# Kernel tuning notes

Hardware: AMD Instinct MI355X
Metric: run time of the kernel (lower is better)

## Reference

```python
import jax, jax.numpy as jnp
import numpy as np
import itertools

# ---- static config (from args) ----
BS = 4; H = 480; W = 640; C = 20
RES = 5; ZRES = 5; MAP_SZ = 480            # map_size_cm//global_downscaling//resolution
VR = 100; FOV = 79.0; NSEM = 16; NC = 1 + NSEM
MAXH = 40; MINH = -8; NZ = MAXH - MINH      # 48 z slices
AGENT_H = 88.0                              # camera_height*100
CAT_T = 5.0; EXP_T = 1.0; MAP_T = 1.0
RADIUS = 30
MIN_Z = int(25 / ZRES - MINH)               # 13
MID_Z = int(AGENT_H / ZRES - MINH)          # 25
MAX_Z = int((AGENT_H + 50) / ZRES - MINH)   # 35
R2D = 57.29577951308232

_F = (W / 2.0) / np.tan(np.deg2rad(FOV / 2.0))
_XC = (W - 1.0) / 2.0
_ZC = (H - 1.0) / 2.0

# circular stair mask (constant)
_ii, _jj = np.meshgrid(np.arange(2 * RADIUS), np.arange(2 * RADIUS), indexing='ij')
STAIR_MASK = jnp.asarray((((_ii + 0.5 - RADIUS) ** 2 + (_jj + 0.5 - RADIUS) ** 2) <= RADIUS ** 2).astype(np.float32))


def affine_grid(theta, Hh, Ww):
    # F.affine_grid, align_corners=False: sample at pixel centers
    xs = (jnp.arange(Ww, dtype=theta.dtype) + 0.5) * 2.0 / Ww - 1.0
    ys = (jnp.arange(Hh, dtype=theta.dtype) + 0.5) * 2.0 / Hh - 1.0
    gx, gy = jnp.meshgrid(xs, ys)  # [H,W]
    base = jnp.stack([gx, gy, jnp.ones_like(gx)], -1)  # [H,W,3]
    return jnp.einsum('hwk,bjk->bhwj', base, theta)    # [B,H,W,2]


def grid_sample(im, grid):
    # F.grid_sample: bilinear, align_corners=True, zeros padding
    B, Cc, Hh, Ww = im.shape
    x = (grid[..., 0] + 1.0) * 0.5 * (Ww - 1)
    y = (grid[..., 1] + 1.0) * 0.5 * (Hh - 1)
    x0 = jnp.floor(x); y0 = jnp.floor(y)

    def gather(ix, iy):
        valid = ((ix >= 0) & (ix < Ww) & (iy >= 0) & (iy < Hh)).astype(im.dtype)
        ixc = jnp.clip(ix, 0, Ww - 1).astype(jnp.int32)
        iyc = jnp.clip(iy, 0, Hh - 1).astype(jnp.int32)
        v = jax.vmap(lambda imb, iyb, ixb: imb[:, iyb, ixb])(im, iyc, ixc)  # [B,C,Hg,Wg]
        return v * valid[:, None, :, :]

    wx = x - x0; wy = y - y0
    return (gather(x0, y0) * ((1 - wx) * (1 - wy))[:, None]
            + gather(x0 + 1, y0) * (wx * (1 - wy))[:, None]
            + gather(x0, y0 + 1) * ((1 - wx) * wy)[:, None]
            + gather(x0 + 1, y0 + 1) * (wx * wy)[:, None])


def splat_feat_nd(feat, coords, dims):
    # trilinear scatter-add splat; feat [B,F,N], coords [B,3,N] in [-1,1]
    B, Fc, N = feat.shape
    G = int(np.prod(dims))
    grid = jnp.zeros((B, Fc, G), feat.dtype)
    pos, wts = [], []
    for d, D in enumerate(dims):
        p = coords[:, d, :] * (D / 2.0) + D / 2.0
        fl = jnp.floor(p)
        pd, wd = [], []
        for ix in (0, 1):
            pix = fl + ix
            safe = ((pix > 0) & (pix < D)).astype(p.dtype)
            wd.append((1.0 - jnp.abs(p - pix)) * safe)
            pd.append(pix * safe)
        pos.append(pd); wts.append(wd)

    def scat(g, idx, val):
        return jax.vmap(lambda gb, ib, vb: gb.at[:, ib].add(vb))(g, idx, val)

    for c0, c1, c2 in itertools.product((0, 1), repeat=3):
        idx = ((pos[0][c0] * dims[1] + pos[1][c1]) * dims[2] + pos[2][c2]).astype(jnp.int32)
        w = wts[0][c0] * wts[1][c1] * wts[2][c2]
        grid = scat(grid, idx, feat * w[:, None, :])
    return jnp.round(grid).reshape(B, Fc, *dims)


def maxpool3(x):  # 3x3 stride1 pad1 max pool, [B,1,H,W]
    return jax.lax.reduce_window(x, -jnp.inf, jax.lax.max, (1, 1, 3, 3), (1, 1, 1, 1), 'SAME')


def _forward(obs, pose_obs, maps_last, poses_last, eve_angle):
    bs, c, h, w = obs.shape
    depth = obs[:, 3]  # [B,H,W], cm

    # point cloud from depth (grid_z flipped top->bottom as in du)
    gx = jnp.arange(w, dtype=obs.dtype)[None, None, :]
    gz = jnp.arange(h - 1, -1, -1, dtype=obs.dtype)[None, :, None]
    X = (gx - _XC) * depth / _F
    Zc = (gz - _ZC) * depth / _F

    # camera elevation rotation about x-axis (per env) + sensor height
    a = jnp.deg2rad(eve_angle)[:, None, None]
    ca, sa = jnp.cos(a), jnp.sin(a)
    Y = ca * depth - sa * Zc
    Z = sa * depth + ca * Zc + AGENT_H
    X = X + VR * RES / 2.0  # shift_loc (rotation angle is 0)

    # normalize to [-1,1] voxel coords
    xs = (X / RES - VR // 2) / VR * 2.0
    ys = (Y / RES - VR // 2) / VR * 2.0
    zs = (Z / ZRES - (MAXH + MINH) // 2) / (MAXH - MINH) * 2.0
    coords = jnp.stack([xs, ys, zs], 1).reshape(bs, 3, h * w)

    feat = jnp.concatenate([jnp.ones((bs, 1, h * w), obs.dtype),
                            obs[:, 4:].reshape(bs, c - 4, h * w)], 1)  # du_scale=1 -> avgpool is identity

    voxels = splat_feat_nd(feat, coords, (VR, VR, NZ)).transpose(0, 1, 3, 2, 4)  # [B,F,y,x,z]

    ahp = voxels[..., MIN_Z:MAX_Z].sum(-1)
    asp = voxels[..., MID_Z - 5:MID_Z].sum(-1)
    allp = voxels.sum(-1)

    fp_map = jnp.clip(ahp[:, 0:1] / MAP_T, 0.0, 1.0)
    fp_stair = jnp.clip(asp[:, 0:1] / MAP_T, 0.0, 1.0)
    fp_exp = jnp.clip(allp[:, 0:1] / EXP_T, 0.0, 1.0)

    x1 = MAP_SZ // 2 - VR // 2; x2 = x1 + VR
    y1 = MAP_SZ // 2; y2 = y1 + VR
    agent_view = jnp.zeros((bs, c, MAP_SZ, MAP_SZ), obs.dtype)
    agent_view = agent_view.at[:, 0:1, y1:y2, x1:x2].set(fp_map)
    agent_view = agent_view.at[:, 1:2, y1:y2, x1:x2].set(fp_exp)
    agent_view = agent_view.at[:, 4:, y1:y2, x1:x2].set(jnp.clip(ahp[:, 1:] / CAT_T, 0.0, 1.0))
    agent_view_stair = jax.lax.stop_gradient(agent_view).at[:, 0:1, y1:y2, x1:x2].set(fp_stair)

    # pose composition (get_new_pose_batch)
    r = poses_last[:, 2] / R2D
    ny = poses_last[:, 1] + pose_obs[:, 0] * jnp.sin(r) + pose_obs[:, 1] * jnp.cos(r)
    nx = poses_last[:, 0] + pose_obs[:, 0] * jnp.cos(r) - pose_obs[:, 1] * jnp.sin(r)
    nt = poses_last[:, 2] + pose_obs[:, 2] * R2D
    nt = jnp.fmod(nt - 180.0, 360.0) + 180.0
    nt = jnp.fmod(nt + 180.0, 360.0) - 180.0
    current_poses = jnp.stack([nx, ny, nt], 1)

    stp = jax.lax.stop_gradient(current_poses)  # st_pose detached in source
    half = MAP_SZ // 2
    sx = (half - stp[:, 0] * 100.0 / RES) / half
    sy = (half - stp[:, 1] * 100.0 / RES) / half
    t = jnp.deg2rad(90.0 - stp[:, 2])
    ct, st = jnp.cos(t), jnp.sin(t)
    zero = jnp.zeros_like(ct); one = jnp.ones_like(ct)
    theta1 = jnp.stack([jnp.stack([ct, -st, zero], 1), jnp.stack([st, ct, zero], 1)], 1)
    theta2 = jnp.stack([jnp.stack([one, zero, sx], 1), jnp.stack([zero, one, sy], 1)], 1)
    rot_grid = affine_grid(theta1, MAP_SZ, MAP_SZ)
    trans_grid = affine_grid(theta2, MAP_SZ, MAP_SZ)

    translated = grid_sample(grid_sample(agent_view, rot_grid), trans_grid)

    diff = translated[:, 1:2] - maxpool3(translated[:, 0:1])
    diff = (diff > 0.8).astype(obs.dtype)
    map_pred = jnp.maximum(maps_last, translated)
    kill = (diff == 1.0) & (eve_angle == 0.0)[:, None, None, None]
    map_pred = map_pred.at[:, 0:1].set(jnp.where(kill, 0.0, map_pred[:, 0:1]))

    translated_stair = grid_sample(grid_sample(agent_view_stair, rot_grid), trans_grid)
    s_x = jnp.clip((current_poses[0, 0] * 100.0 / 5.0).astype(jnp.int32), RADIUS, MAP_SZ - RADIUS - 1)
    s_y = jnp.clip((current_poses[0, 1] * 100.0 / 5.0).astype(jnp.int32), RADIUS, MAP_SZ - RADIUS - 1)
    stair_grid = jax.lax.dynamic_update_slice(jnp.zeros((MAP_SZ, MAP_SZ), obs.dtype), STAIR_MASK,
                                              (s_y - RADIUS, s_x - RADIUS))
    translated_stair = translated_stair.at[0, 0:2].multiply(stair_grid[None])

    diff_s = translated_stair[:, 1:2] - translated_stair[:, 0:1]
    diff_s = (diff_s > 0.8).astype(obs.dtype)
    map_pred_stair = jnp.maximum(maps_last, translated_stair)
    kill_s = (diff_s == 1.0) & (eve_angle == 0.0)[:, None, None, None]
    map_pred_stair = map_pred_stair.at[:, 0:1].set(jnp.where(kill_s, 0.0, map_pred_stair[:, 0:1]))

    return translated, map_pred, map_pred_stair, current_poses


def setup_inputs() -> dict:
    key = jax.random.key(0)
    k1, k2, k3, k4, k5 = jax.random.split(key, 5)
    obs = jax.random.uniform(k1, (BS, C, H, W), jnp.float32)
    depth = jax.random.uniform(k2, (BS, H, W), jnp.float32) * 400.0 + 50.0  # cm
    obs = obs.at[:, 3].set(depth)
    pose_obs = (jax.random.uniform(k3, (BS, 3), jnp.float32) - 0.5) * 0.2   # small rel pose (m, m, rad)
    maps_last = jax.random.uniform(k4, (BS, C, MAP_SZ, MAP_SZ), jnp.float32)
    poses_last = jnp.tile(jnp.array([12.0, 12.0, 0.0], jnp.float32), (BS, 1)) \
        + (jax.random.uniform(k5, (BS, 3), jnp.float32) - 0.5) * jnp.array([2.0, 2.0, 60.0], jnp.float32)
    eve_angle = jnp.array([0.0, -30.0, 0.0, 30.0], jnp.float32)
    return {"obs": obs, "pose_obs": pose_obs, "maps_last": maps_last,
            "poses_last": poses_last, "eve_angle": eve_angle}


def reference(obs, pose_obs, maps_last, poses_last, eve_angle):
    return _forward(obs, pose_obs, maps_last, poses_last, eve_angle)
```

## Files before the change

kernel.cpp:

```cpp
#include <hip/hip_runtime.h>
#include <math.h>

#define BS 4
#define NCH 20
#define IMH 480
#define IMW 640
#define NPIX (IMH*IMW)
#define MSZ 480
#define MPX (MSZ*MSZ)
#define VR 100

#define TX 5
#define TY 8
#define NRX 20
#define NRY 13
#define NBIN (NRX*NRY)
#define CELLS (TX*TY)
#define CELLF 401

#define WND 176
#define NT  11

#define FPSCALE 65536.0f
#define FPINV   (1.0f/65536.0f)
#define SEMSCALE 65535.0f
#define SEMINV   (1.0f/65535.0f)

#define FCONST 388.19028f
#define D2R    0.017453292519943295f
#define R2DF   57.29577951308232f

typedef float    fx4  __attribute__((ext_vector_type(4)));
typedef unsigned ux4  __attribute__((ext_vector_type(4)));

static constexpr size_t SEG = (size_t)BS*NCH*MPX;
static constexpr size_t SEMT_FLOATS = (size_t)BS*NPIX*8;
static constexpr size_t LIST_CAP    = (size_t)4*BS*NPIX;
static constexpr size_t LIST_OFF_OUT = SEMT_FLOATS;
static_assert(LIST_OFF_OUT + LIST_CAP < 2*SEG, "semT+list must fit in out0+out1 segments");

static constexpr size_t OFF_AV     = 0;
static constexpr size_t OFF_AVS    = 720000;
static constexpr size_t OFF_COUNTS = 1681664;
static constexpr size_t OFF_CURS   = 1682704;
static constexpr size_t OFF_OFFS   = 1683744;
static constexpr size_t OFF_SEMT   = 1684800;
static constexpr size_t OFF_LIST   = OFF_SEMT + SEMT_FLOATS;
static constexpr size_t WS_NEED_B  = (OFF_LIST + LIST_CAP) * 4;

__device__ __forceinline__ float clip01(float v) { return fminf(fmaxf(v, 0.0f), 1.0f); }

struct Geo { float px, py, pz; };

__device__ __forceinline__ Geo geom(int p, float depth, float ca, float sa) {
  int j = p % IMW;
  int i = p / IMW;
  float dF = depth * (1.0f / FCONST);
  float X  = ((float)j - 319.5f) * dF;
  X += 250.0f;
  float gz = (float)(IMH - 1 - i);
  float Zc = (gz - 239.5f) * dF;
  float Y  = ca*depth - sa*Zc;
  float Z  = sa*depth + ca*Zc + 88.0f;
  float xs = (X/5.0f - 50.0f)/100.0f*2.0f;
  float ys = (Y/5.0f - 50.0f)/100.0f*2.0f;
  float zs = (Z/5.0f - 16.0f)/48.0f*2.0f;
  Geo g;
  g.px = xs*50.0f + 50.0f;
  g.py = ys*50.0f + 50.0f;
  g.pz = zs*24.0f + 24.0f;
  return g;
}

__device__ __forceinline__ int pixel_bins(Geo g, int bins[4]) {
  float fx = floorf(g.px), fy = floorf(g.py), fz = floorf(g.pz);
  float fx1 = fx + 1.0f, fy1 = fy + 1.0f, fz1 = fz + 1.0f;
  bool vx0 = (fx  > 0.0f) && (fx  < 100.0f);
  bool vx1 = (fx1 > 0.0f) && (fx1 < 100.0f);
  bool vy0 = (fy  > 0.0f) && (fy  < 100.0f);
  bool vy1 = (fy1 > 0.0f) && (fy1 < 100.0f);
  bool vz0 = (fz  > 0.0f) && (fz  < 48.0f);
  bool vz1 = (fz1 > 0.0f) && (fz1 < 48.0f);
  if (!((vx0||vx1) && (vy0||vy1) && (vz0||vz1))) return 0;
  int rxs[2]; int nx = 0;
  if (vx0) rxs[nx++] = (int)fx / TX;
  if (vx1) { int r = (int)fx1 / TX; if (!nx || r != rxs[0]) rxs[nx++] = r; }
  int rys[2]; int ny = 0;
  if (vy0) rys[ny++] = (int)fy / TY;
  if (vy1) { int r = (int)fy1 / TY; if (!ny || r != rys[0]) rys[ny++] = r; }
  int n = 0;
  for (int a = 0; a < ny; ++a)
    for (int c = 0; c < nx; ++c)
      bins[n++] = rys[a]*NRX + rxs[c];
  return n;
}

__device__ __forceinline__ void pose_calc(const float* __restrict__ pose_obs,
                                          const float* __restrict__ poses_last,
                                          int b, float& nx, float& ny, float& nt) {
  float pl0 = poses_last[b*3+0], pl1 = poses_last[b*3+1], pl2 = poses_last[b*3+2];
  float po0 = pose_obs[b*3+0],   po1 = pose_obs[b*3+1],   po2 = pose_obs[b*3+2];
  float r  = pl2 / R2DF;
  float sr = sinf(r), cr = cosf(r);
  ny = pl1 + po0*sr + po1*cr;
  nx = pl0 + po0*cr - po1*sr;
  nt = pl2 + po2*R2DF;
  nt = fmodf(nt - 180.0f, 360.0f) + 180.0f;
  nt = fmodf(nt + 180.0f, 360.0f) - 180.0f;
}

__global__ __launch_bounds__(256) void k_prep(const float* __restrict__ obs,
                                              const float* __restrict__ pose_obs,
                                              const float* __restrict__ poses_last,
                                              const float* __restrict__ eve,
                                              unsigned* __restrict__ counts,
                                              unsigned short* __restrict__ semT,
                                              float* __restrict__ out_poses) {
  __shared__ unsigned hist[NBIN];
  int tid = threadIdx.x;
  int b   = blockIdx.y;
  if (blockIdx.x == 0 && b == 0 && tid < BS) {
    float nx, ny, nt;
    pose_calc(pose_obs, poses_last, tid, nx, ny, nt);
    out_poses[tid*3+0] = nx;
    out_poses[tid*3+1] = ny;
    out_poses[tid*3+2] = nt;
  }
  for (int i = tid; i < NBIN; i += 256) hist[i] = 0u;
  __syncthreads();
  float a  = eve[b] * D2R;
  float ca = cosf(a), sa = sinf(a);
  const float* __restrict__ dpl  = obs + ((size_t)b*NCH + 3)*NPIX;
  const float* __restrict__ semb = obs + ((size_t)b*NCH + 4)*NPIX;
  int base = blockIdx.x * 2048;
#pragma unroll
  for (int k = 0; k < 8; ++k) {
    int p = base + k*256 + tid;
    Geo g = geom(p, dpl[p], ca, sa);
    int bins[4];
    int n = pixel_bins(g, bins);
    for (int t = 0; t < n; ++t) atomicAdd(&hist[bins[t]], 1u);
    bool wantSem = false;
    if (n > 0) {
      float fz = floorf(g.pz);
#pragma unroll
      for (int kk = 0; kk < 2; ++kk) {
        float pv = fz + (float)kk;
        if (pv > 0.0f && pv < 48.0f) {
          int zv = (int)pv;
          if (zv >= 13 && zv < 35) wantSem = true;
        }
      }
    }
    if (wantSem) {
      unsigned u[8];
#pragma unroll
      for (int k2 = 0; k2 < 8; ++k2) {
        float s0 = semb[(size_t)(2*k2  )*NPIX + p];
        float s1 = semb[(size_t)(2*k2+1)*NPIX + p];
        unsigned q0 = (unsigned)(clip01(s0)*SEMSCALE + 0.5f);
        unsigned q1 = (unsigned)(clip01(s1)*SEMSCALE + 0.5f);
        u[k2] = q0 | (q1 << 16);
      }
      ux4* dst = (ux4*)(semT + ((size_t)b*NPIX + p)*16);
      ux4 v0 = {u[0], u[1], u[2], u[3]};
      ux4 v1 = {u[4], u[5], u[6], u[7]};
      __builtin_nontemporal_store(v0, dst);
      __builtin_nontemporal_store(v1, dst + 1);
    }
  }
  __syncthreads();
  for (int i = tid; i < NBIN; i += 256) {
    unsigned v = hist[i];
    if (v) atomicAdd(&counts[b*NBIN + i], v);
  }
}

__global__ __launch_bounds__(256) void k_scatter(const float* __restrict__ obs,
                                                 const float* __restrict__ eve,
                                                 const unsigned* __restrict__ counts,
                                                 unsigned* __restrict__ curs,
                                                 unsigned* __restrict__ offs_g,
                                                 unsigned* __restrict__ list) {
  __shared__ unsigned hist[NBIN];
  __shared__ unsigned lbase[NBIN];
  __shared__ unsigned slot[NBIN];
  __shared__ unsigned offsL[BS*NBIN];
  __shared__ unsigned partial[256];
  int tid = threadIdx.x;
  int b   = blockIdx.y;
  for (int i = tid; i < NBIN; i += 256) { hist[i] = 0u; slot[i] = 0u; }
  {
    unsigned loc[5]; unsigned s = 0;
#pragma unroll
    for (int k = 0; k < 5; ++k) {
      int idx = tid*5 + k;
      unsigned v = (idx < BS*NBIN) ? counts[idx] : 0u;
      loc[k] = s; s += v;
    }
    partial[tid] = s;
    __syncthreads();
    for (int off = 1; off < 256; off <<= 1) {
      unsigned v = (tid >= off) ? partial[tid - off] : 0u;
      __syncthreads();
      partial[tid] += v;
      __syncthreads();
    }
    unsigned base = (tid > 0) ? partial[tid-1] : 0u;
#pragma unroll
    for (int k = 0; k < 5; ++k) {
      int idx = tid*5 + k;
      if (idx < BS*NBIN) offsL[idx] = base + loc[k];
    }
    __syncthreads();
  }
  if (blockIdx.x == 0 && b == 0)
    for (int i = tid; i < BS*NBIN; i += 256) offs_g[i] = offsL[i];

  float a  = eve[b] * D2R;
  float ca = cosf(a), sa = sinf(a);
  const float* __restrict__ dpl = obs + ((size_t)b*NCH + 3)*NPIX;
  int base = blockIdx.x * 2048;
#pragma unroll
  for (int k = 0; k < 8; ++k) {
    int p = base + k*256 + tid;
    Geo g = geom(p, dpl[p], ca, sa);
    int bins[4];
    int n = pixel_bins(g, bins);
    for (int t = 0; t < n; ++t) atomicAdd(&hist[bins[t]], 1u);
  }
  __syncthreads();
  for (int i = tid; i < NBIN; i += 256) {
    unsigned h = hist[i];
    lbase[i] = h ? (offsL[b*NBIN + i] + atomicAdd(&curs[b*NBIN + i], h)) : 0u;
  }
  __syncthreads();
#pragma unroll
  for (int k = 0; k < 8; ++k) {
    int p = base + k*256 + tid;
    Geo g = geom(p, dpl[p], ca, sa);
    int bins[4];
    int n = pixel_bins(g, bins);
    for (int t = 0; t < n; ++t) {
      int bn = bins[t];
      unsigned sidx = atomicAdd(&slot[bn], 1u);
      list[lbase[bn] + sidx] = (unsigned)p;
    }
  }
}

__global__ __launch_bounds__(1024) void k_splat_fast(const float* __restrict__ obs,
                                                     const unsigned short* __restrict__ semT,
                                                     const float* __restrict__ eve,
                                                     const unsigned* __restrict__ offs,
                                                     const unsigned* __restrict__ counts,
                                                     const unsigned* __restrict__ list,
                                                     float* __restrict__ av,
                                                     float* __restrict__ avs,
                                                     const float* __restrict__ maps_last,
                                                     float* __restrict__ out0,
                                                     float* __restrict__ out1,
                                                     float* __restrict__ out2,
                                                     int nSplat, int nFast) {
  __shared__ unsigned lds[CELLS * CELLF];
  const int bid = blockIdx.x;
  const int tid = threadIdx.x;

  if (bid >= nSplat) {
    const size_t n4 = SEG/4;
    const size_t stride = (size_t)nFast * 1024;
    const fx4* __restrict__ m4 = (const fx4*)maps_last;
    fx4 z4 = {0.0f, 0.0f, 0.0f, 0.0f};
    for (size_t i = (size_t)(bid - nSplat) * 1024 + tid; i < n4; i += stride) {
      fx4 m = __builtin_nontemporal_load(m4 + i);
      fx4 r;
      r.x = fmaxf(m.x, 0.0f); r.y = fmaxf(m.y, 0.0f);
      r.z = fmaxf(m.z, 0.0f); r.w = fmaxf(m.w, 0.0f);
      __builtin_nontemporal_store(z4, (fx4*)out0 + i);
      __builtin_nontemporal_store(r,  (fx4*)out1 + i);
      __builtin_nontemporal_store(r,  (fx4*)out2 + i);
    }
    return;
  }

  const int reg = bid % NBIN;
  const int b   = bid / NBIN;
  const int rx0 = (reg % NRX) * TX;
  const int ry0 = (reg / NRX) * TY;

  for (int i = tid; i < CELLS * CELLF; i += 1024) lds[i] = 0u;
  __syncthreads();

  float aa = eve[b] * D2R;
  float ca = cosf(aa), sa = sinf(aa);
  const float* __restrict__ dpl = obs + ((size_t)b*NCH + 3)*NPIX;

  const unsigned bin   = (unsigned)b*NBIN + reg;
  const unsigned start = offs[bin];
  const unsigned n     = counts[bin];

  for (unsigned ii = tid; ii < n; ii += 1024) {
    int p = (int)list[start + ii];
    Geo g = geom(p, dpl[p], ca, sa);
    float px = g.px, py = g.py, pz = g.pz;
    float fx = floorf(px), fy = floorf(py), fz = floorf(pz);

    float wxa[2], wya[2], wza[2];
    int   ixa[2], iya[2], iza[2];
    bool  vx[2], vy[2], vz[2];
#pragma unroll
    for (int k = 0; k < 2; ++k) {
      float pv = fx + (float)k;
      bool sg = (pv > 0.0f) && (pv < 100.0f);
      wxa[k] = sg ? (1.0f - fabsf(px - pv)) : 0.0f;
      ixa[k] = (int)pv;
      vx[k]  = sg && (ixa[k] >= rx0) && (ixa[k] < rx0 + TX);

      pv = fy + (float)k;
      sg = (pv > 0.0f) && (pv < 100.0f);
      wya[k] = sg ? (1.0f - fabsf(py - pv)) : 0.0f;
      iya[k] = (int)pv;
      vy[k]  = sg && (iya[k] >= ry0) && (iya[k] < ry0 + TY);

      pv = fz + (float)k;
      sg = (pv > 0.0f) && (pv < 48.0f);
      wza[k] = sg ? (1.0f - fabsf(pz - pv)) : 0.0f;
      iza[k] = (int)pv;
      vz[k]  = sg;
    }

    bool needSem = false;
#pragma unroll
    for (int k = 0; k < 2; ++k)
      if (vz[k] && iza[k] >= 13 && iza[k] < 35 && wza[k] != 0.0f) needSem = true;

    float sem[16];
    if (needSem) {
      const ux4* sp = (const ux4*)(semT + ((size_t)b*NPIX + p)*16);
      ux4 a4 = sp[0], b4 = sp[1];
      sem[0]  = (float)(a4.x & 0xffffu); sem[1]  = (float)(a4.x >> 16);
      sem[2]  = (float)(a4.y & 0xffffu); sem[3]  = (float)(a4.y >> 16);
      sem[4]  = (float)(a4.z & 0xffffu); sem[5]  = (float)(a4.z >> 16);
      sem[6]  = (float)(a4.w & 0xffffu); sem[7]  = (float)(a4.w >> 16);
      sem[8]  = (float)(b4.x & 0xffffu); sem[9]  = (float)(b4.x >> 16);
      sem[10] = (float)(b4.y & 0xffffu); sem[11] = (float)(b4.y >> 16);
      sem[12] = (float)(b4.z & 0xffffu); sem[13] = (float)(b4.z >> 16);
      sem[14] = (float)(b4.w & 0xffffu); sem[15] = (float)(b4.w >> 16);
    }

#pragma unroll
    for (int cx = 0; cx < 2; ++cx) {
      if (!vx[cx] || wxa[cx] == 0.0f) continue;
#pragma unroll
      for (int cy = 0; cy < 2; ++cy) {
        if (!vy[cy]) continue;
        float wxy = wxa[cx] * wya[cy];
        if (wxy == 0.0f) continue;
        unsigned* cellp = lds + (size_t)((ixa[cx]-rx0)*TY + (iya[cy]-ry0)) * CELLF;
#pragma unroll
        for (int cz = 0; cz < 2; ++cz) {
          if (!vz[cz]) continue;
          float wv = wxy * wza[cz];
          if (wv == 0.0f) continue;
          int zv = iza[cz];
          atomicAdd(cellp + zv, (unsigned)(wv*FPSCALE + 0.5f));
          if (zv >= 13 && zv < 35) {
            unsigned* p2 = cellp + 48 + (zv - 13)*16;
#pragma unroll
            for (int c = 0; c < 16; ++c)
              atomicAdd(p2 + c, (unsigned)(wv*sem[c] + 0.5f));
          }
        }
      }
    }
  }
  __syncthreads();

  for (int it = tid; it < CELLS * 17; it += 1024) {
    int cell = it % CELLS;
    int ch   = it / CELLS;
    int lx = cell / TY, ly = cell % TY;
    int x = rx0 + lx, y = ry0 + ly;
    if (y >= 100) continue;
    size_t pxo = (size_t)y*VR + x;
    size_t ab  = (size_t)b*18*10000;
    const unsigned* cellp = lds + (size_t)cell * CELLF;
    if (ch == 0) {
      float all0 = 0.0f, ahp0 = 0.0f, asp0 = 0.0f;
#pragma unroll
      for (int z = 0; z < 48; ++z) {
        float v = rintf((float)cellp[z] * FPINV);
        all0 += v;
        if (z >= 13 && z < 35) ahp0 += v;
        if (z >= 20 && z < 25) asp0 += v;
      }
      av[ab + 0*10000 + pxo] = clip01(ahp0);
      av[ab + 1*10000 + pxo] = clip01(all0);
      avs[(size_t)b*10000 + pxo] = clip01(asp0);
    } else {
      int c = ch - 1;
      float acc = 0.0f;
      for (int z = 0; z < 22; ++z) acc += rintf((float)cellp[48 + z*16 + c] * SEMINV);
      av[ab + (size_t)(2 + c)*10000 + pxo] = clip01(acc / 5.0f);
    }
  }
}

__global__ __launch_bounds__(256) void k_fast(const float* __restrict__ maps_last,
                                              float* __restrict__ out0,
                                              float* __restrict__ out1,
                                              float* __restrict__ out2) {
  const size_t n4 = SEG/4;
  const size_t stride = (size_t)gridDim.x * 256;
  const fx4* __restrict__ m4 = (const fx4*)maps_last;
  fx4 z4 = {0.0f, 0.0f, 0.0f, 0.0f};
  for (size_t i = (size_t)blockIdx.x * 256 + threadIdx.x; i < n4; i += stride) {
    fx4 m = __builtin_nontemporal_load(m4 + i);
    fx4 r;
    r.x = fmaxf(m.x, 0.0f); r.y = fmaxf(m.y, 0.0f);
    r.z = fmaxf(m.z, 0.0f); r.w = fmaxf(m.w, 0.0f);
    __builtin_nontemporal_store(z4, (fx4*)out0 + i);
    __builtin_nontemporal_store(r,  (fx4*)out1 + i);
    __builtin_nontemporal_store(r,  (fx4*)out2 + i);
  }
}

struct Nb { float wt, w00, w10, w01, w11; int o00, o10, o01, o11; };

__device__ __forceinline__ Nb rot_taps(int xi, int yi, float ct, float st, float wt) {
  Nb nb; nb.wt = 0.0f;
  nb.w00 = nb.w10 = nb.w01 = nb.w11 = 0.0f;
  nb.o00 = nb.o10 = nb.o01 = nb.o11 = 0;
  if (xi < 0 || xi >= MSZ || yi < 0 || yi >= MSZ) return nb;
  float gx = ((xi + 0.5f)*2.0f)/480.0f - 1.0f;
  float gy = ((yi + 0.5f)*2.0f)/480.0f - 1.0f;
  float u = gx*ct - gy*st;
  float v = gx*st + gy*ct;
  float xf = (u + 1.0f)*0.5f*479.0f;
  float yf = (v + 1.0f)*0.5f*479.0f;
  float x0f = floorf(xf), y0f = floorf(yf);
  int x0 = (int)x0f, y0 = (int)y0f;
  if (x0 < 189 || x0 > 289 || y0 < 239 || y0 > 339) return nb;
  float wx = xf - x0f, wy = yf - y0f;
  bool vx0 = (x0   >= 190) && (x0   < 290);
  bool vx1 = (x0+1 >= 190) && (x0+1 < 290);
  bool vy0 = (y0   >= 240) && (y0   < 340);
  bool vy1 = (y0+1 >= 240) && (y0+1 < 340);
  int base = (y0-240)*100 + (x0-190);
  bool v00 = vx0&&vy0, v10 = vx1&&vy0, v01 = vx0&&vy1, v11 = vx1&&vy1;
  nb.w00 = v00 ? (1.0f-wx)*(1.0f-wy) : 0.0f;  nb.o00 = v00 ? base       : 0;
  nb.w10 = v10 ? wx*(1.0f-wy)        : 0.0f;  nb.o10 = v10 ? base + 1   : 0;
  nb.w01 = v01 ? (1.0f-wx)*wy        : 0.0f;  nb.o01 = v01 ? base + 100 : 0;
  nb.w11 = v11 ? wx*wy               : 0.0f;  nb.o11 = v11 ? base + 101 : 0;
  nb.wt  = wt;
  return nb;
}

__device__ __forceinline__ bool trans_nbs(int w, int h, float sx, float sy,
                                          float ct, float st, Nb nb[4]) {
#pragma unroll
  for (int i = 0; i < 4; ++i) {
    nb[i].wt = 0.0f;
    nb[i].w00 = nb[i].w10 = nb[i].w01 = nb[i].w11 = 0.0f;
    nb[i].o00 = nb[i].o10 = nb[i].o01 = nb[i].o11 = 0;
  }
  float gx = ((w + 0.5f)*2.0f)/480.0f - 1.0f;
  float gy = ((h + 0.5f)*2.0f)/480.0f - 1.0f;
  float xf = ((gx + sx) + 1.0f)*0.5f*479.0f;
  float yf = ((gy + sy) + 1.0f)*0.5f*479.0f;
  float x0f = floorf(xf), y0f = floorf(yf);
  int x0 = (int)x0f, y0 = (int)y0f;
  if (x0 < -1 || x0 > 479 || y0 < -1 || y0 > 479) return false;
  float wx = xf - x0f, wy = yf - y0f;
  nb[0] = rot_taps(x0,   y0,   ct, st, (1.0f-wx)*(1.0f-wy));
  nb[1] = rot_taps(x0+1, y0,   ct, st, wx*(1.0f-wy));
  nb[2] = rot_taps(x0,   y0+1, ct, st, (1.0f-wx)*wy);
  nb[3] = rot_taps(x0+1, y0+1, ct, st, wx*wy);
  return (nb[0].wt!=0.0f)||(nb[1].wt!=0.0f)||(nb[2].wt!=0.0f)||(nb[3].wt!=0.0f);
}

__device__ __forceinline__ float eval_plane(const float* __restrict__ plane, const Nb nb[4]) {
  float t = 0.0f;
#pragma unroll
  for (int i = 0; i < 4; ++i) {
    if (nb[i].wt == 0.0f) continue;
    float r = plane[nb[i].o00]*nb[i].w00 + plane[nb[i].o10]*nb[i].w10
            + plane[nb[i].o01]*nb[i].w01 + plane[nb[i].o11]*nb[i].w11;
    t += nb[i].wt * r;
  }
  return t;
}

#define TILE 16
__global__ __launch_bounds__(256) void k_heavy(const float* __restrict__ av,
                                               const float* __restrict__ avs,
                                               const float* __restrict__ pose_obs,
                                               const float* __restrict__ poses_last,
                                               const float* __restrict__ eve,
                                               const float* __restrict__ maps_last,
                                               float* __restrict__ out0,
                                               float* __restrict__ out1,
                                               float* __restrict__ out2) {
  __shared__ float t0s[18][19];
  const int b = blockIdx.y;

  float nx, ny, nt;
  pose_calc(pose_obs, poses_last, b, nx, ny, nt);
  float t2 = (90.0f - nt) * D2R;
  const float ct = cosf(t2), st = sinf(t2);
  const float sx = (240.0f - nx*100.0f/5.0f) / 240.0f;
  const float sy = (240.0f - ny*100.0f/5.0f) / 240.0f;
  const bool eve0 = (eve[b] == 0.0f);
  int wx0, wy0;
  {
    const float u_lo = 189.0f/239.5f - 1.0f, u_hi = 290.0f/239.5f - 1.0f;
    const float v_lo = 239.0f/239.5f - 1.0f, v_hi = 340.0f/239.5f - 1.0f;
    float ximin = 1e9f, yimin = 1e9f;
#pragma unroll
    for (int k = 0; k < 4; ++k) {
      float uu = (k & 1) ? u_hi : u_lo;
      float vv = (k & 2) ? v_hi : v_lo;
      float gxc =  uu*ct + vv*st;
      float gyc = -uu*st + vv*ct;
      float xi = (gxc + 1.0f)*240.0f - 0.5f;
      float yi = (gyc + 1.0f)*240.0f - 0.5f;
      ximin = fminf(ximin, xi);
      yimin = fminf(yimin, yi);
    }
    float wmin = 240.0f*((ximin - 1.0f)/239.5f - sx) - 0.5f;
    float hmin = 240.0f*((yimin - 1.0f)/239.5f - sy) - 0.5f;
    wx0 = min(max((int)floorf(wmin) - 3, 0), MSZ - WND);
    wy0 = min(max((int)floorf(hmin) - 3, 0), MSZ - WND);
  }
  int sxi = 0, syi = 0;
  if (b == 0) {
    float nx0, ny0, nt0;
    pose_calc(pose_obs, poses_last, 0, nx0, ny0, nt0);
    sxi = min(max((int)(nx0 * 100.0f / 5.0f), 30), 449);
    syi = min(max((int)(ny0 * 100.0f / 5.0f), 30), 449);
  }

  const int tx0 = wx0 + (blockIdx.x % NT) * TILE;
  const int ty0 = wy0 + (blockIdx.x / NT) * TILE;
  const int lx  = threadIdx.x % TILE;
  const int ly  = threadIdx.x / TILE;
  const float* __restrict__ av0 = av + (size_t)b*18*10000;

  for (int q = threadIdx.x; q < 18*18; q += 256) {
    int hy = q / 18, hx = q % 18;
    int h = ty0 + hy - 1, w = tx0 + hx - 1;
    float v;
    if (h < 0 || h >= MSZ || w < 0 || w >= MSZ) {
      v = -INFINITY;
    } else {
      Nb nb[4];
      v = trans_nbs(w, h, sx, sy, ct, st, nb) ? eval_plane(av0, nb) : 0.0f;
    }
    t0s[hy][hx] = v;
  }
  __syncthreads();

  const int h = ty0 + ly, w = tx0 + lx;
  const size_t pix = (size_t)h*MSZ + w;

  float mp = -INFINITY;
#pragma unroll
  for (int dy = 0; dy < 3; ++dy)
#pragma unroll
    for (int dx = 0; dx < 3; ++dx)
      mp = fmaxf(mp, t0s[ly+dy][lx+dx]);
  float t0 = t0s[ly+1][lx+1];

  Nb nb[4];
  bool hit = trans_nbs(w, h, sx, sy, ct, st, nb);

  float t[19];
  t[0] = t0;
  if (hit) {
#pragma unroll
    for (int s = 1; s < 18; ++s) t[s] = eval_plane(av0 + (size_t)s*10000, nb);
    t[18] = eval_plane(avs + (size_t)b*10000, nb);
  } else {
#pragma unroll
    for (int s = 1; s < 19; ++s) t[s] = 0.0f;
  }

  float t1v = t[1];
  bool kill = ((t1v - mp) > 0.8f) && eve0;

  float sg = 1.0f;
  if (b == 0) {
    int di = h - (syi - 30);
    int dj = w - (sxi - 30);
    if (di >= 0 && di < 60 && dj >= 0 && dj < 60) {
      float aa = (float)di - 29.5f;
      float bb = (float)dj - 29.5f;
      sg = (aa*aa + bb*bb <= 900.0f) ? 1.0f : 0.0f;
    } else {
      sg = 0.0f;
    }
  }
  float tsv0 = t[18] * sg;
  float ts1  = t1v * sg;
  bool kill_s = ((ts1 - tsv0) > 0.8f) && eve0;

  const float* ML = maps_last + (size_t)b*NCH*MPX;
  float* O0 = out0 + (size_t)b*NCH*MPX;
  float* O1 = out1 + (size_t)b*NCH*MPX;
  float* O2 = out2 + (size_t)b*NCH*MPX;

#pragma unroll
  for (int c = 0; c < NCH; ++c) {
    float tv  = (c == 0) ? t0 : ((c == 1) ? t1v : ((c < 4) ? 0.0f : t[c - 2]));
    float tsv = (c == 0) ? tsv0 : ((c == 1) ? ts1 : tv);
    float ml  = ML[(size_t)c*MPX + pix];
    float mpv = fmaxf(ml, tv);
    float msv = fmaxf(ml, tsv);
    if (c == 0) {
      if (kill)   mpv = 0.0f;
      if (kill_s) msv = 0.0f;
    }
    O0[(size_t)c*MPX + pix] = tv;
    O1[(size_t)c*MPX + pix] = mpv;
    O2[(size_t)c*MPX + pix] = msv;
  }
}

extern "C" void kernel_launch(void* const* d_in, const int* in_sizes, int n_in,
                              void* d_out, int out_size, void* d_ws, size_t ws_size,
                              hipStream_t stream) {
  (void)in_sizes; (void)n_in; (void)out_size;
  const float* obs        = (const float*)d_in[0];
  const float* pose_obs   = (const float*)d_in[1];
  const float* maps_last  = (const float*)d_in[2];
  const float* poses_last = (const float*)d_in[3];
  const float* eve        = (const float*)d_in[4];
  float* out = (float*)d_out;
  float* ws  = (float*)d_ws;

  float*    av     = ws + OFF_AV;
  float*    avs    = ws + OFF_AVS;
  unsigned* counts = (unsigned*)(ws + OFF_COUNTS);
  unsigned* curs   = (unsigned*)(ws + OFF_CURS);
  unsigned* offs   = (unsigned*)(ws + OFF_OFFS);

  float* out0 = out;
  float* out1 = out + SEG;
  float* out2 = out + 2*SEG;
  float* outp = out + 3*SEG;

  const bool big_ws = (ws_size >= WS_NEED_B);
  unsigned short* semT = big_ws ? (unsigned short*)(ws + OFF_SEMT)
                                : (unsigned short*)out0;
  unsigned*       list = big_ws ? (unsigned*)(ws + OFF_LIST)
                                : (unsigned*)(out + LIST_OFF_OUT);

  hipMemsetAsync(counts, 0, 2*BS*NBIN*sizeof(unsigned), stream);
  {
    dim3 g(NPIX/2048, BS);
    k_prep<<<g, 256, 0, stream>>>(obs, pose_obs, poses_last, eve, counts, semT, outp);
    k_scatter<<<g, 256, 0, stream>>>(obs, eve, counts, curs, offs, list);
  }
  {
    const int nSplat = NBIN*BS;
    const int nFast  = big_ws ? 1024 : 0;
    k_splat_fast<<<nSplat + nFast, 1024, 0, stream>>>(obs, semT, eve, offs, counts, list,
                                                      av, avs, maps_last, out0, out1, out2,
                                                      nSplat, nFast);
  }
  if (!big_ws) {
    k_fast<<<2048, 256, 0, stream>>>(maps_last, out0, out1, out2);
  }
  {
    dim3 g(NT*NT, BS);
    k_heavy<<<g, 256, 0, stream>>>(av, avs, pose_obs, poses_last, eve, maps_last, out0, out1, out2);
  }
}
```

Baseline: 221.0 us.

## Move map copy into scatter kernel and make splat persistent with work stealing

The bandwidth-bound maps_last relu/zero copy blocks now ride along with the scatter kernel instead of the splat kernel. The splat kernel becomes a persistent grid of 512 blocks that pull bins from a global atomic counter, so heavily populated bins are balanced across blocks. The aim is to overlap the streaming copy with the lighter scatter pass and to reduce tail imbalance in the splat. The cost is an extra atomic counter, which is zeroed by a widened memset, plus extra synchronisation per bin iteration, and the copy now competes with scatter for bandwidth.

```diff
diff --git a/kernel.cpp b/kernel.cpp
--- a/kernel.cpp
+++ b/kernel.cpp
@@ -15,6 +15,7 @@
 #define NRX 20
 #define NRY 13
 #define NBIN (NRX*NRY)
+#define NBINT (BS*NBIN)
 #define CELLS (TX*TY)
 #define CELLF 401
 
@@ -43,7 +44,8 @@
 static constexpr size_t OFF_AVS    = 720000;
 static constexpr size_t OFF_COUNTS = 1681664;
 static constexpr size_t OFF_CURS   = 1682704;
-static constexpr size_t OFF_OFFS   = 1683744;
+static constexpr size_t OFF_WSTEAL = 1683744;
+static constexpr size_t OFF_OFFS   = 1683760;
 static constexpr size_t OFF_SEMT   = 1684800;
 static constexpr size_t OFF_LIST   = OFF_SEMT + SEMT_FLOATS;
 static constexpr size_t WS_NEED_B  = (OFF_LIST + LIST_CAP) * 4;
@@ -176,26 +178,51 @@
   }
 }
 
-__global__ __launch_bounds__(256) void k_scatter(const float* __restrict__ obs,
-                                                 const float* __restrict__ eve,
-                                                 const unsigned* __restrict__ counts,
-                                                 unsigned* __restrict__ curs,
-                                                 unsigned* __restrict__ offs_g,
-                                                 unsigned* __restrict__ list) {
+__global__ __launch_bounds__(256) void k_scatter_fast(const float* __restrict__ obs,
+                                                      const float* __restrict__ eve,
+                                                      const unsigned* __restrict__ counts,
+                                                      unsigned* __restrict__ curs,
+                                                      unsigned* __restrict__ offs_g,
+                                                      unsigned* __restrict__ list,
+                                                      const float* __restrict__ maps_last,
+                                                      float* __restrict__ out0,
+                                                      float* __restrict__ out1,
+                                                      float* __restrict__ out2,
+                                                      int nScatter, int nFast) {
   __shared__ unsigned hist[NBIN];
   __shared__ unsigned lbase[NBIN];
   __shared__ unsigned slot[NBIN];
-  __shared__ unsigned offsL[BS*NBIN];
+  __shared__ unsigned offsL[NBINT];
   __shared__ unsigned partial[256];
-  int tid = threadIdx.x;
-  int b   = blockIdx.y;
+  const int bid = blockIdx.x;
+  const int tid = threadIdx.x;
+
+  if (bid >= nScatter) {
+    const size_t n4 = SEG/4;
+    const size_t stride = (size_t)nFast * 256;
+    const fx4* __restrict__ m4 = (const fx4*)maps_last;
+    fx4 z4 = {0.0f, 0.0f, 0.0f, 0.0f};
+    for (size_t i = (size_t)(bid - nScatter) * 256 + tid; i < n4; i += stride) {
+      fx4 m = __builtin_nontemporal_load(m4 + i);
+      fx4 r;
+      r.x = fmaxf(m.x, 0.0f); r.y = fmaxf(m.y, 0.0f);
+      r.z = fmaxf(m.z, 0.0f); r.w = fmaxf(m.w, 0.0f);
+      __builtin_nontemporal_store(z4, (fx4*)out0 + i);
+      __builtin_nontemporal_store(r,  (fx4*)out1 + i);
+      __builtin_nontemporal_store(r,  (fx4*)out2 + i);
+    }
+    return;
+  }
+
+  const int xblk = bid % (NPIX/2048);
+  const int b    = bid / (NPIX/2048);
   for (int i = tid; i < NBIN; i += 256) { hist[i] = 0u; slot[i] = 0u; }
   {
     unsigned loc[5]; unsigned s = 0;
 #pragma unroll
     for (int k = 0; k < 5; ++k) {
       int idx = tid*5 + k;
-      unsigned v = (idx < BS*NBIN) ? counts[idx] : 0u;
+      unsigned v = (idx < NBINT) ? counts[idx] : 0u;
       loc[k] = s; s += v;
     }
     partial[tid] = s;
@@ -210,17 +237,17 @@
 #pragma unroll
     for (int k = 0; k < 5; ++k) {
       int idx = tid*5 + k;
-      if (idx < BS*NBIN) offsL[idx] = base + loc[k];
+      if (idx < NBINT) offsL[idx] = base + loc[k];
     }
     __syncthreads();
   }
-  if (blockIdx.x == 0 && b == 0)
-    for (int i = tid; i < BS*NBIN; i += 256) offs_g[i] = offsL[i];
+  if (bid == 0)
+    for (int i = tid; i < NBINT; i += 256) offs_g[i] = offsL[i];
 
   float a  = eve[b] * D2R;
   float ca = cosf(a), sa = sinf(a);
   const float* __restrict__ dpl = obs + ((size_t)b*NCH + 3)*NPIX;
-  int base = blockIdx.x * 2048;
+  int base = xblk * 2048;
 #pragma unroll
   for (int k = 0; k < 8; ++k) {
     int p = base + k*256 + tid;
@@ -249,160 +276,146 @@
   }
 }
 
-__global__ __launch_bounds__(1024) void k_splat_fast(const float* __restrict__ obs,
-                                                     const unsigned short* __restrict__ semT,
-                                                     const float* __restrict__ eve,
-                                                     const unsigned* __restrict__ offs,
-                                                     const unsigned* __restrict__ counts,
-                                                     const unsigned* __restrict__ list,
-                                                     float* __restrict__ av,
-                                                     float* __restrict__ avs,
-                                                     const float* __restrict__ maps_last,
-                                                     float* __restrict__ out0,
-                                                     float* __restrict__ out1,
-                                                     float* __restrict__ out2,
-                                                     int nSplat, int nFast) {
+__global__ __launch_bounds__(1024) void k_splat(const float* __restrict__ obs,
+                                                const unsigned short* __restrict__ semT,
+                                                const float* __restrict__ eve,
+                                                const unsigned* __restrict__ offs,
+                                                const unsigned* __restrict__ counts,
+                                                const unsigned* __restrict__ list,
+                                                unsigned* __restrict__ wsteal,
+                                                float* __restrict__ av,
+                                                float* __restrict__ avs) {
   __shared__ unsigned lds[CELLS * CELLF];
-  const int bid = blockIdx.x;
+  __shared__ unsigned binShared;
   const int tid = threadIdx.x;
 
-  if (bid >= nSplat) {
-    const size_t n4 = SEG/4;
-    const size_t stride = (size_t)nFast * 1024;
-    const fx4* __restrict__ m4 = (const fx4*)maps_last;
-    fx4 z4 = {0.0f, 0.0f, 0.0f, 0.0f};
-    for (size_t i = (size_t)(bid - nSplat) * 1024 + tid; i < n4; i += stride) {
-      fx4 m = __builtin_nontemporal_load(m4 + i);
-      fx4 r;
-      r.x = fmaxf(m.x, 0.0f); r.y = fmaxf(m.y, 0.0f);
-      r.z = fmaxf(m.z, 0.0f); r.w = fmaxf(m.w, 0.0f);
-      __builtin_nontemporal_store(z4, (fx4*)out0 + i);
-      __builtin_nontemporal_store(r,  (fx4*)out1 + i);
-      __builtin_nontemporal_store(r,  (fx4*)out2 + i);
-    }
-    return;
-  }
-
-  const int reg = bid % NBIN;
-  const int b   = bid / NBIN;
-  const int rx0 = (reg % NRX) * TX;
-  const int ry0 = (reg / NRX) * TY;
-
-  for (int i = tid; i < CELLS * CELLF; i += 1024) lds[i] = 0u;
-  __syncthreads();
-
-  float aa = eve[b] * D2R;
-  float ca = cosf(aa), sa = sinf(aa);
-  const float* __restrict__ dpl = obs + ((size_t)b*NCH + 3)*NPIX;
-
-  const unsigned bin   = (unsigned)b*NBIN + reg;
-  const unsigned start = offs[bin];
-  const unsigned n     = counts[bin];
-
-  for (unsigned ii = tid; ii < n; ii += 1024) {
-    int p = (int)list[start + ii];
-    Geo g = geom(p, dpl[p], ca, sa);
-    float px = g.px, py = g.py, pz = g.pz;
-    float fx = floorf(px), fy = floorf(py), fz = floorf(pz);
-
-    float wxa[2], wya[2], wza[2];
-    int   ixa[2], iya[2], iza[2];
-    bool  vx[2], vy[2], vz[2];
-#pragma unroll
-    for (int k = 0; k < 2; ++k) {
-      float pv = fx + (float)k;
-      bool sg = (pv > 0.0f) && (pv < 100.0f);
-      wxa[k] = sg ? (1.0f - fabsf(px - pv)) : 0.0f;
-      ixa[k] = (int)pv;
-      vx[k]  = sg && (ixa[k] >= rx0) && (ixa[k] < rx0 + TX);
-
-      pv = fy + (float)k;
-      sg = (pv > 0.0f) && (pv < 100.0f);
-      wya[k] = sg ? (1.0f - fabsf(py - pv)) : 0.0f;
-      iya[k] = (int)pv;
-      vy[k]  = sg && (iya[k] >= ry0) && (iya[k] < ry0 + TY);
-
-      pv = fz + (float)k;
-      sg = (pv > 0.0f) && (pv < 48.0f);
-      wza[k] = sg ? (1.0f - fabsf(pz - pv)) : 0.0f;
-      iza[k] = (int)pv;
-      vz[k]  = sg;
-    }
-
-    bool needSem = false;
-#pragma unroll
-    for (int k = 0; k < 2; ++k)
-      if (vz[k] && iza[k] >= 13 && iza[k] < 35 && wza[k] != 0.0f) needSem = true;
-
-    float sem[16];
-    if (needSem) {
-      const ux4* sp = (const ux4*)(semT + ((size_t)b*NPIX + p)*16);
-      ux4 a4 = sp[0], b4 = sp[1];
-      sem[0]  = (float)(a4.x & 0xffffu); sem[1]  = (float)(a4.x >> 16);
-      sem[2]  = (float)(a4.y & 0xffffu); sem[3]  = (float)(a4.y >> 16);
-      sem[4]  = (float)(a4.z & 0xffffu); sem[5]  = (float)(a4.z >> 16);
-      sem[6]  = (float)(a4.w & 0xffffu); sem[7]  = (float)(a4.w >> 16);
-      sem[8]  = (float)(b4.x & 0xffffu); sem[9]  = (float)(b4.x >> 16);
-      sem[10] = (float)(b4.y & 0xffffu); sem[11] = (float)(b4.y >> 16);
-      sem[12] = (float)(b4.z & 0xffffu); sem[13] = (float)(b4.z >> 16);
-      sem[14] = (float)(b4.w & 0xffffu); sem[15] = (float)(b4.w >> 16);
-    }
-
-#pragma unroll
-    for (int cx = 0; cx < 2; ++cx) {
-      if (!vx[cx] || wxa[cx] == 0.0f) continue;
-#pragma unroll
-      for (int cy = 0; cy < 2; ++cy) {
-        if (!vy[cy]) continue;
-        float wxy = wxa[cx] * wya[cy];
-        if (wxy == 0.0f) continue;
-        unsigned* cellp = lds + (size_t)((ixa[cx]-rx0)*TY + (iya[cy]-ry0)) * CELLF;
-#pragma unroll
-        for (int cz = 0; cz < 2; ++cz) {
-          if (!vz[cz]) continue;
-          float wv = wxy * wza[cz];
-          if (wv == 0.0f) continue;
-          int zv = iza[cz];
-          atomicAdd(cellp + zv, (unsigned)(wv*FPSCALE + 0.5f));
-          if (zv >= 13 && zv < 35) {
-            unsigned* p2 = cellp + 48 + (zv - 13)*16;
-#pragma unroll
-            for (int c = 0; c < 16; ++c)
-              atomicAdd(p2 + c, (unsigned)(wv*sem[c] + 0.5f));
+  for (;;) {
+    if (tid == 0) binShared = atomicAdd(wsteal, 1u);
+    __syncthreads();
+    const unsigned mybin = binShared;
+    if (mybin >= (unsigned)NBINT) break;
+
+    const int reg = (int)(mybin % NBIN);
+    const int b   = (int)(mybin / NBIN);
+    const int rx0 = (reg % NRX) * TX;
+    const int ry0 = (reg / NRX) * TY;
+
+    for (int i = tid; i < CELLS * CELLF; i += 1024) lds[i] = 0u;
+    __syncthreads();
+
+    float aa = eve[b] * D2R;
+    float ca = cosf(aa), sa = sinf(aa);
+    const float* __restrict__ dpl = obs + ((size_t)b*NCH + 3)*NPIX;
+
+    const unsigned start = offs[mybin];
+    const unsigned n     = counts[mybin];
+
+    for (unsigned ii = tid; ii < n; ii += 1024) {
+      int p = (int)list[start + ii];
+      Geo g = geom(p, dpl[p], ca, sa);
+      float px = g.px, py = g.py, pz = g.pz;
+      float fx = floorf(px), fy = floorf(py), fz = floorf(pz);
+
+      float wxa[2], wya[2], wza[2];
+      int   ixa[2], iya[2], iza[2];
+      bool  vx[2], vy[2], vz[2];
+#pragma unroll
+      for (int k = 0; k < 2; ++k) {
+        float pv = fx + (float)k;
+        bool sg = (pv > 0.0f) && (pv < 100.0f);
+        wxa[k] = sg ? (1.0f - fabsf(px - pv)) : 0.0f;
+        ixa[k] = (int)pv;
+        vx[k]  = sg && (ixa[k] >= rx0) && (ixa[k] < rx0 + TX);
+
+        pv = fy + (float)k;
+        sg = (pv > 0.0f) && (pv < 100.0f);
+        wya[k] = sg ? (1.0f - fabsf(py - pv)) : 0.0f;
+        iya[k] = (int)pv;
+        vy[k]  = sg && (iya[k] >= ry0) && (iya[k] < ry0 + TY);
+
+        pv = fz + (float)k;
+        sg = (pv > 0.0f) && (pv < 48.0f);
+        wza[k] = sg ? (1.0f - fabsf(pz - pv)) : 0.0f;
+        iza[k] = (int)pv;
+        vz[k]  = sg;
+      }
+
+      bool needSem = false;
+#pragma unroll
+      for (int k = 0; k < 2; ++k)
+        if (vz[k] && iza[k] >= 13 && iza[k] < 35 && wza[k] != 0.0f) needSem = true;
+
+      float sem[16];
+      if (needSem) {
+        const ux4* sp = (const ux4*)(semT + ((size_t)b*NPIX + p)*16);
+        ux4 a4 = sp[0], b4 = sp[1];
+        sem[0]  = (float)(a4.x & 0xffffu); sem[1]  = (float)(a4.x >> 16);
+        sem[2]  = (float)(a4.y & 0xffffu); sem[3]  = (float)(a4.y >> 16);
+        sem[4]  = (float)(a4.z & 0xffffu); sem[5]  = (float)(a4.z >> 16);
+        sem[6]  = (float)(a4.w & 0xffffu); sem[7]  = (float)(a4.w >> 16);
+        sem[8]  = (float)(b4.x & 0xffffu); sem[9]  = (float)(b4.x >> 16);
+        sem[10] = (float)(b4.y & 0xffffu); sem[11] = (float)(b4.y >> 16);
+        sem[12] = (float)(b4.z & 0xffffu); sem[13] = (float)(b4.z >> 16);
+        sem[14] = (float)(b4.w & 0xffffu); sem[15] = (float)(b4.w >> 16);
+      }
+
+#pragma unroll
+      for (int cx = 0; cx < 2; ++cx) {
+        if (!vx[cx] || wxa[cx] == 0.0f) continue;
+#pragma unroll
+        for (int cy = 0; cy < 2; ++cy) {
+          if (!vy[cy]) continue;
+          float wxy = wxa[cx] * wya[cy];
+          if (wxy == 0.0f) continue;
+          unsigned* cellp = lds + (size_t)((ixa[cx]-rx0)*TY + (iya[cy]-ry0)) * CELLF;
+#pragma unroll
+          for (int cz = 0; cz < 2; ++cz) {
+            if (!vz[cz]) continue;
+            float wv = wxy * wza[cz];
+            if (wv == 0.0f) continue;
+            int zv = iza[cz];
+            atomicAdd(cellp + zv, (unsigned)(wv*FPSCALE + 0.5f));
+            if (zv >= 13 && zv < 35) {
+              unsigned* p2 = cellp + 48 + (zv - 13)*16;
+#pragma unroll
+              for (int c = 0; c < 16; ++c)
+                atomicAdd(p2 + c, (unsigned)(wv*sem[c] + 0.5f));
+            }
           }
         }
       }
     }
-  }
-  __syncthreads();
-
-  for (int it = tid; it < CELLS * 17; it += 1024) {
-    int cell = it % CELLS;
-    int ch   = it / CELLS;
-    int lx = cell / TY, ly = cell % TY;
-    int x = rx0 + lx, y = ry0 + ly;
-    if (y >= 100) continue;
-    size_t pxo = (size_t)y*VR + x;
-    size_t ab  = (size_t)b*18*10000;
-    const unsigned* cellp = lds + (size_t)cell * CELLF;
-    if (ch == 0) {
-      float all0 = 0.0f, ahp0 = 0.0f, asp0 = 0.0f;
-#pragma unroll
-      for (int z = 0; z < 48; ++z) {
-        float v = rintf((float)cellp[z] * FPINV);
-        all0 += v;
-        if (z >= 13 && z < 35) ahp0 += v;
-        if (z >= 20 && z < 25) asp0 += v;
+    __syncthreads();
+
+    for (int it = tid; it < CELLS * 17; it += 1024) {
+      int cell = it % CELLS;
+      int ch   = it / CELLS;
+      int lx = cell / TY, ly = cell % TY;
+      int x = rx0 + lx, y = ry0 + ly;
+      if (y >= 100) continue;
+      size_t pxo = (size_t)y*VR + x;
+      size_t ab  = (size_t)b*18*10000;
+      const unsigned* cellp = lds + (size_t)cell * CELLF;
+      if (ch == 0) {
+        float all0 = 0.0f, ahp0 = 0.0f, asp0 = 0.0f;
+#pragma unroll
+        for (int z = 0; z < 48; ++z) {
+          float v = rintf((float)cellp[z] * FPINV);
+          all0 += v;
+          if (z >= 13 && z < 35) ahp0 += v;
+          if (z >= 20 && z < 25) asp0 += v;
+        }
+        av[ab + 0*10000 + pxo] = clip01(ahp0);
+        av[ab + 1*10000 + pxo] = clip01(all0);
+        avs[(size_t)b*10000 + pxo] = clip01(asp0);
+      } else {
+        int c = ch - 1;
+        float acc = 0.0f;
+        for (int z = 0; z < 22; ++z) acc += rintf((float)cellp[48 + z*16 + c] * SEMINV);
+        av[ab + (size_t)(2 + c)*10000 + pxo] = clip01(acc / 5.0f);
       }
-      av[ab + 0*10000 + pxo] = clip01(ahp0);
-      av[ab + 1*10000 + pxo] = clip01(all0);
-      avs[(size_t)b*10000 + pxo] = clip01(asp0);
-    } else {
-      int c = ch - 1;
-      float acc = 0.0f;
-      for (int z = 0; z < 22; ++z) acc += rintf((float)cellp[48 + z*16 + c] * SEMINV);
-      av[ab + (size_t)(2 + c)*10000 + pxo] = clip01(acc / 5.0f);
-    }
+    }
+    __syncthreads();
   }
 }
 
@@ -642,6 +655,7 @@
   float*    avs    = ws + OFF_AVS;
   unsigned* counts = (unsigned*)(ws + OFF_COUNTS);
   unsigned* curs   = (unsigned*)(ws + OFF_CURS);
+  unsigned* wsteal = (unsigned*)(ws + OFF_WSTEAL);
   unsigned* offs   = (unsigned*)(ws + OFF_OFFS);
 
   float* out0 = out;
@@ -655,19 +669,19 @@
   unsigned*       list = big_ws ? (unsigned*)(ws + OFF_LIST)
                                 : (unsigned*)(out + LIST_OFF_OUT);
 
-  hipMemsetAsync(counts, 0, 2*BS*NBIN*sizeof(unsigned), stream);
+  hipMemsetAsync(counts, 0, (2*NBINT + 16)*sizeof(unsigned), stream);
   {
     dim3 g(NPIX/2048, BS);
     k_prep<<<g, 256, 0, stream>>>(obs, pose_obs, poses_last, eve, counts, semT, outp);
-    k_scatter<<<g, 256, 0, stream>>>(obs, eve, counts, curs, offs, list);
   }
   {
-    const int nSplat = NBIN*BS;
-    const int nFast  = big_ws ? 1024 : 0;
-    k_splat_fast<<<nSplat + nFast, 1024, 0, stream>>>(obs, semT, eve, offs, counts, list,
-                                                      av, avs, maps_last, out0, out1, out2,
-                                                      nSplat, nFast);
-  }
+    const int nScatter = (NPIX/2048) * BS;
+    const int nFast    = big_ws ? 1024 : 0;
+    k_scatter_fast<<<nScatter + nFast, 256, 0, stream>>>(obs, eve, counts, curs, offs, list,
+                                                         maps_last, out0, out1, out2,
+                                                         nScatter, nFast);
+  }
+  k_splat<<<512, 1024, 0, stream>>>(obs, semT, eve, offs, counts, list, wsteal, av, avs);
   if (!big_ws) {
     k_fast<<<2048, 256, 0, stream>>>(maps_last, out0, out1, out2);
   }
```

After: 291.7 us. 32.0% more time.
